# Kernel optimization log

Measured on AMD Instinct MI355X. Metric: run time of the kernel, lower is better.

The kernel has to match this reference:

```python
import jax, jax.numpy as jnp
import numpy as np

V = 50257      # vocab_size
EMB = 300      # emb_size
H = 512        # mcan_flat_out_size (GRU hidden)
HS = 256       # hidden_size (object proposal feature dim)
BH = 256       # bi_hidden_size (encoder output feature dim)
NP = 256       # num_proposal
ML = 50        # max_length (lang seq len)
AL = 20        # answer length -> 19 decode steps
NEG = -1e9


def setup_inputs() -> dict:
    key = jax.random.key(0)
    ks = jax.random.split(key, 30)
    s = 0.02
    n = lambda k, sh: (s * jax.random.normal(k, sh)).astype(jnp.float32)
    d = {}
    d["input_tok"] = jax.random.randint(ks[0], (1,), 0, V, dtype=jnp.int32)
    d["hidden"] = jax.random.normal(ks[1], (1, 1, H), jnp.float32)
    d["encoder_outputs"] = jax.random.normal(ks[2], (ML, BH), jnp.float32)
    d["object_proposals"] = jax.random.normal(ks[3], (NP, HS), jnp.float32)
    d["object_mask"] = jax.random.randint(ks[4], (1, NP), 0, 2, dtype=jnp.int32)
    d["lang_mask"] = jax.random.randint(ks[5], (1, ML), 0, 2, dtype=jnp.int32)
    d["answer_to_vocab"] = jax.random.randint(ks[6], (AL,), 0, V, dtype=jnp.int32)
    # learned params (dropout treated as eval/identity)
    d["emb"] = n(ks[7], (V, EMB))
    cin = H + EMB  # 812
    d["attn_w1"] = n(ks[8], (256, cin)); d["attn_b1"] = jnp.zeros((256,), jnp.float32)
    d["attn_w2"] = n(ks[9], (ML, 256)); d["attn_b2"] = jnp.zeros((ML,), jnp.float32)
    d["attn_op_w1"] = n(ks[10], (256, cin)); d["attn_op_b1"] = jnp.zeros((256,), jnp.float32)
    d["attn_op_w2"] = n(ks[11], (NP, 256)); d["attn_op_b2"] = jnp.zeros((NP,), jnp.float32)
    comb_in = HS + BH + EMB  # 812
    d["cmb_w1"] = n(ks[12], (512, comb_in)); d["cmb_b1"] = jnp.zeros((512,), jnp.float32)
    d["cmb_w2"] = n(ks[13], (H, 512)); d["cmb_b2"] = jnp.zeros((H,), jnp.float32)
    d["gru_w_ih"] = n(ks[14], (3 * H, H)); d["gru_w_hh"] = n(ks[15], (3 * H, H))
    d["gru_b_ih"] = jnp.zeros((3 * H,), jnp.float32); d["gru_b_hh"] = jnp.zeros((3 * H,), jnp.float32)
    d["out_w"] = n(ks[16], (V, H)); d["out_b"] = jnp.zeros((V,), jnp.float32)
    return d


def reference(input_tok, hidden, encoder_outputs, object_proposals, object_mask,
              lang_mask, answer_to_vocab, emb, attn_w1, attn_b1, attn_w2, attn_b2,
              attn_op_w1, attn_op_b1, attn_op_w2, attn_op_b2, cmb_w1, cmb_b1,
              cmb_w2, cmb_b2, gru_w_ih, gru_w_hh, gru_b_ih, gru_b_hh, out_w, out_b):
    obj_m = object_mask.astype(bool)   # [1, NP]
    lang_m = lang_mask.astype(bool)    # [1, ML]
    # teacher forcing: step i embeds answer_to_vocab[i] (step 0 uses input_tok)
    tokens = jnp.concatenate([input_tok, answer_to_vocab[1:-1]])  # [AL-1]

    def step(h, tok):
        # h: [1,1,H]
        x = jax.nn.relu(emb[tok])[None, :]                     # [1,EMB]
        cat = jnp.concatenate([x, h[0]], axis=1)               # [1, EMB+H]
        # object attention
        a_op = jax.nn.relu(cat @ attn_op_w1.T + attn_op_b1) @ attn_op_w2.T + attn_op_b2
        a_op = jax.nn.softmax(jnp.where(obj_m, NEG, a_op), axis=1)   # [1,NP]
        ctx_op = a_op @ object_proposals                       # [1,HS]
        # language attention
        a_l = jax.nn.relu(cat @ attn_w1.T + attn_b1) @ attn_w2.T + attn_b2
        a_l = jax.nn.softmax(jnp.where(lang_m, NEG, a_l), axis=1)    # [1,ML]
        ctx = a_l @ encoder_outputs                            # [1,BH]
        comb = jnp.concatenate([x, ctx, ctx_op], axis=1)       # [1, EMB+BH+HS]
        g = jax.nn.relu(jax.nn.relu(comb @ cmb_w1.T + cmb_b1) @ cmb_w2.T + cmb_b2)  # [1,H]
        # GRU cell (torch gate order: r, z, n)
        gi = g @ gru_w_ih.T + gru_b_ih
        gh = h[0] @ gru_w_hh.T + gru_b_hh
        i_r, i_z, i_n = jnp.split(gi, 3, axis=1)
        h_r, h_z, h_n = jnp.split(gh, 3, axis=1)
        r = jax.nn.sigmoid(i_r + h_r)
        z = jax.nn.sigmoid(i_z + h_z)
        nn_ = jnp.tanh(i_n + r * h_n)
        h_new = (1.0 - z) * nn_ + z * h[0]                     # [1,H]
        logits = h_new @ out_w.T + out_b                       # [1,V]
        return h_new[None], (logits, a_l, a_op)

    _, (logits, attn_w, attn_ob_w) = jax.lax.scan(step, hidden, tokens)
    # logits: [AL-1,1,V]; attn_w: [AL-1,1,ML]; attn_ob_w: [AL-1,1,NP]
    return logits, attn_w, attn_ob_w
```

## Files before the change

### kernel.cpp

```cpp
#include <hip/hip_runtime.h>
#include <math.h>

#define T_STEPS 19
#define V 50257
#define EMB 300
#define HDIM 512
#define NP 256
#define ML 50
#define CIN 812
#define NEGV -1e9f
#define NBLK 64

#define OFF_X      0
#define OFF_POP    5700
#define OFF_PL     10564
#define OFF_PC     15428
#define OFF_HS     25156
#define OFF_H1OP   35396
#define OFF_H1L    35652
#define OFF_C1     35908
#define OFF_G      36420
#define OFF_LOGOP  36932
#define OFF_LOGL   37188
#define OFF_MPROP  37252
#define OFF_MENC   168324
#define OFF_BAR    193924

#define OUT_LOGITS 0
#define OUT_ATTW   ((long)T_STEPS * V)
#define OUT_ATTOB  (OUT_ATTW + (long)T_STEPS * ML)

__device__ __forceinline__ float wred(float v) {
  v += __shfl_xor(v, 32, 64);
  v += __shfl_xor(v, 16, 64);
  v += __shfl_xor(v, 8, 64);
  v += __shfl_xor(v, 4, 64);
  v += __shfl_xor(v, 2, 64);
  v += __shfl_xor(v, 1, 64);
  return v;
}

__device__ __forceinline__ float dot4(float4 a, float4 b) {
  return a.x * b.x + a.y * b.y + a.z * b.z + a.w * b.w;
}

__device__ __forceinline__ void gstore(float* p, float v) {
  __hip_atomic_store(p, v, __ATOMIC_RELAXED, __HIP_MEMORY_SCOPE_AGENT);
}
__device__ __forceinline__ float ld1c(const float* p) {
  return __hip_atomic_load(p, __ATOMIC_RELAXED, __HIP_MEMORY_SCOPE_AGENT);
}
__device__ __forceinline__ float2 ld2c(const float* p) {
  unsigned long long u = __hip_atomic_load((const unsigned long long*)p,
                                           __ATOMIC_RELAXED, __HIP_MEMORY_SCOPE_AGENT);
  float2 r;
  r.x = __uint_as_float((unsigned)u);
  r.y = __uint_as_float((unsigned)(u >> 32));
  return r;
}
__device__ __forceinline__ float4 ld4c(const float* p) {
  float2 a = ld2c(p), b = ld2c(p + 2);
  return make_float4(a.x, a.y, b.x, b.y);
}

__device__ __forceinline__ void gbar(float* wsb, unsigned bar) {
  asm volatile("s_waitcnt vmcnt(0)" ::: "memory");
  __syncthreads();
  unsigned* flags = (unsigned*)(wsb + OFF_BAR) + 16;
  if (threadIdx.x == 0) {
    __hip_atomic_store(flags + 16 * blockIdx.x, bar, __ATOMIC_RELAXED, __HIP_MEMORY_SCOPE_AGENT);
  }
  asm volatile("" ::: "memory");
  if (threadIdx.x < 64) {
    unsigned* f = flags + 16 * threadIdx.x;
    while (__hip_atomic_load(f, __ATOMIC_RELAXED, __HIP_MEMORY_SCOPE_AGENT) < bar) {
      __builtin_amdgcn_s_sleep(1);
    }
  }
  __syncthreads();
}

__global__ void k_pre1(const int* __restrict__ tok0, const int* __restrict__ ans,
                       const float* __restrict__ emb, const float* __restrict__ hidden,
                       float* __restrict__ ws) {
  int tid = blockIdx.x * 256 + threadIdx.x;
  if (tid < T_STEPS * EMB) {
    int s = tid / EMB, j = tid - s * EMB;
    int t = (s == 0) ? tok0[0] : ans[s];
    float v = emb[(long)t * EMB + j];
    ws[OFF_X + tid] = v > 0.f ? v : 0.f;
  } else {
    int k = tid - T_STEPS * EMB;
    if (k < HDIM) ws[OFF_HS + k] = hidden[k];
  }
}

__global__ void k_pre2(const float* __restrict__ w1op, const float* __restrict__ b1op,
                       const float* __restrict__ w1l,  const float* __restrict__ b1l,
                       const float* __restrict__ wc1,  const float* __restrict__ bc1,
                       float* __restrict__ ws) {
  int gw = (blockIdx.x * 256 + threadIdx.x) >> 6;
  int lane = threadIdx.x & 63;
  int s = gw >> 10;
  int rr = gw & 1023;
  if (s >= T_STEPS) return;
  const float* wrow; const float* bias; float* dst; int r;
  if (rr < 256)      { r = rr;       wrow = w1op + (long)r * CIN; bias = b1op; dst = ws + OFF_POP + s * 256 + r; }
  else if (rr < 512) { r = rr - 256; wrow = w1l  + (long)r * CIN; bias = b1l;  dst = ws + OFF_PL  + s * 256 + r; }
  else               { r = rr - 512; wrow = wc1  + (long)r * CIN; bias = bc1;  dst = ws + OFF_PC  + s * 512 + r; }
  const float* x = ws + OFF_X + s * EMB;
  float acc = 0.f;
#pragma unroll
  for (int it = 0; it < 5; ++it) {
    int j = it * 64 + lane;
    if (j < EMB) acc += wrow[j] * x[j];
  }
  acc = wred(acc);
  if (lane == 0) *dst = acc + bias[r];
}

#define LDSF 12850
__global__ void __launch_bounds__(256) k_mprep(const float* __restrict__ cw1,
                                               const float* __restrict__ prop,
                                               const float* __restrict__ enc,
                                               float* __restrict__ ws) {
  __shared__ float lds[LDSF];
  int tid = threadIdx.x, r = blockIdx.x;
  float acc = 0.f;
  for (int kc = 0; kc < 8; ++kc) {
    __syncthreads();
#pragma unroll
    for (int i = 0; i < 8; ++i) {
      int f = tid + 256 * i; int row = f >> 3, q = f & 7;
      float4 v = *(const float4*)(prop + (long)row * 256 + kc * 32 + 4 * q);
      float* p = lds + row * 33 + 4 * q;
      p[0] = v.x; p[1] = v.y; p[2] = v.z; p[3] = v.w;
    }
    __syncthreads();
    const float* wbase = cw1 + (long)r * CIN + 556 + kc * 32;
    const float* pl = lds + tid * 33;
#pragma unroll
    for (int k4 = 0; k4 < 8; ++k4) {
      float4 w4 = *(const float4*)(wbase + 4 * k4);
      const float* pp = pl + 4 * k4;
      acc += w4.x * pp[0] + w4.y * pp[1] + w4.z * pp[2] + w4.w * pp[3];
    }
  }
  ws[OFF_MPROP + (long)r * 256 + tid] = acc;
  __syncthreads();
  for (int i = 0; i < 13; ++i) {
    int f = tid + 256 * i;
    if (f < 3200) {
      int row = f >> 6, q = f & 63;
      float4 v = *(const float4*)(enc + (long)row * 256 + 4 * q);
      float* p = lds + row * 257 + 4 * q;
      p[0] = v.x; p[1] = v.y; p[2] = v.z; p[3] = v.w;
    }
  }
  __syncthreads();
  if (tid < ML) {
    const float* wb2 = cw1 + (long)r * CIN + 300;
    const float* el = lds + tid * 257;
    float a2 = 0.f;
#pragma unroll 8
    for (int k = 0; k < 256; ++k) a2 += wb2[k] * el[k];
    ws[OFF_MENC + (long)r * ML + tid] = a2;
  }
}

__global__ void __launch_bounds__(256, 1) k_recur(
    const float* __restrict__ w1op, const float* __restrict__ w1l,
    const float* __restrict__ whh,  const float* __restrict__ bhh,
    const float* __restrict__ w2op, const float* __restrict__ b2op,
    const float* __restrict__ w2l,  const float* __restrict__ b2l,
    const int* __restrict__ obj_mask, const int* __restrict__ lang_mask,
    const float* __restrict__ wc2,  const float* __restrict__ bc2,
    const float* __restrict__ wih,  const float* __restrict__ bih,
    float* ws, float* __restrict__ out) {
  const int tid = threadIdx.x;
  const int lane = tid & 63;
  const int wv = (blockIdx.x << 2) + (tid >> 6);
  const int r0 = 2 * wv, r1 = 2 * wv + 1;
  const int l4 = 4 * lane;
  unsigned bar = 1;
  __shared__ float red[256];
  __shared__ __align__(16) float sm_aop[256];
  __shared__ float sm_al[64];

  const float* wa0p = (r0 < 256) ? (w1op + (long)r0 * CIN + 300) : (w1l + (long)(r0 - 256) * CIN + 300);
  const float* wa1p = (r1 < 256) ? (w1op + (long)r1 * CIN + 300) : (w1l + (long)(r1 - 256) * CIN + 300);
  float4 WA00 = *(const float4*)(wa0p + l4), WA01 = *(const float4*)(wa0p + 256 + l4);
  float4 WA10 = *(const float4*)(wa1p + l4), WA11 = *(const float4*)(wa1p + 256 + l4);
  const float* q;
  q = whh + (long)r0 * HDIM;           float4 WH00 = *(const float4*)(q + l4), WH01 = *(const float4*)(q + 256 + l4);
  q = whh + (long)(r0 + 512) * HDIM;   float4 WH10 = *(const float4*)(q + l4), WH11 = *(const float4*)(q + 256 + l4);
  q = whh + (long)(r0 + 1024) * HDIM;  float4 WH20 = *(const float4*)(q + l4), WH21 = *(const float4*)(q + 256 + l4);
  q = whh + (long)r1 * HDIM;           float4 WH30 = *(const float4*)(q + l4), WH31 = *(const float4*)(q + 256 + l4);
  q = whh + (long)(r1 + 512) * HDIM;   float4 WH40 = *(const float4*)(q + l4), WH41 = *(const float4*)(q + 256 + l4);
  q = whh + (long)(r1 + 1024) * HDIM;  float4 WH50 = *(const float4*)(q + l4), WH51 = *(const float4*)(q + 256 + l4);
  float4 W2  = *(const float4*)(w2op + (long)wv * 256 + l4);
  float4 W2L = (wv < ML) ? *(const float4*)(w2l + (long)wv * 256 + l4) : make_float4(0.f, 0.f, 0.f, 0.f);
  float4 MP0 = *(const float4*)(ws + OFF_MPROP + (long)r0 * 256 + l4);
  float4 MP1 = *(const float4*)(ws + OFF_MPROP + (long)r1 * 256 + l4);
  float  ME0 = (lane < ML) ? ws[OFF_MENC + (long)r0 * ML + lane] : 0.f;
  float  ME1 = (lane < ML) ? ws[OFF_MENC + (long)r1 * ML + lane] : 0.f;
  q = wc2 + (long)r0 * HDIM;           float4 WC00 = *(const float4*)(q + l4), WC01 = *(const float4*)(q + 256 + l4);
  q = wc2 + (long)r1 * HDIM;           float4 WC10 = *(const float4*)(q + l4), WC11 = *(const float4*)(q + 256 + l4);
  q = wih + (long)r0 * HDIM;           float4 WI00 = *(const float4*)(q + l4), WI01 = *(const float4*)(q + 256 + l4);
  q = wih + (long)(r0 + 512) * HDIM;   float4 WI10 = *(const float4*)(q + l4), WI11 = *(const float4*)(q + 256 + l4);
  q = wih + (long)(r0 + 1024) * HDIM;  float4 WI20 = *(const float4*)(q + l4), WI21 = *(const float4*)(q + 256 + l4);
  q = wih + (long)r1 * HDIM;           float4 WI30 = *(const float4*)(q + l4), WI31 = *(const float4*)(q + 256 + l4);
  q = wih + (long)(r1 + 512) * HDIM;   float4 WI40 = *(const float4*)(q + l4), WI41 = *(const float4*)(q + 256 + l4);
  q = wih + (long)(r1 + 1024) * HDIM;  float4 WI50 = *(const float4*)(q + l4), WI51 = *(const float4*)(q + 256 + l4);
  float BH0 = bhh[r0], BH1 = bhh[512 + r0], BH2 = bhh[1024 + r0];
  float BH3 = bhh[r1], BH4 = bhh[512 + r1], BH5 = bhh[1024 + r1];
  float BI0 = bih[r0], BI1 = bih[512 + r0], BI2 = bih[1024 + r0];
  float BI3 = bih[r1], BI4 = bih[512 + r1], BI5 = bih[1024 + r1];
  float BC0 = bc2[r0], BC1 = bc2[r1];
  float B2  = b2op[wv];
  float B2Lv = (wv < ML) ? b2l[wv] : 0.f;

  for (int s = 0; s < T_STEPS; ++s) {
    float ghr0, ghz0, ghn0, ghr1, ghz1, ghn1;
    {
      const float* h = ws + OFF_HS + s * HDIM;
      float4 ha = ld4c(h + l4);
      float4 hb = ld4c(h + 256 + l4);
      float a0 = dot4(WA00, ha) + dot4(WA01, hb);
      float a1 = dot4(WA10, ha) + dot4(WA11, hb);
      float b0 = dot4(WH00, ha) + dot4(WH01, hb);
      float b1 = dot4(WH10, ha) + dot4(WH11, hb);
      float b2 = dot4(WH20, ha) + dot4(WH21, hb);
      float b3 = dot4(WH30, ha) + dot4(WH31, hb);
      float b4 = dot4(WH40, ha) + dot4(WH41, hb);
      float b5 = dot4(WH50, ha) + dot4(WH51, hb);
      a0 = wred(a0); a1 = wred(a1);
      b0 = wred(b0); b1 = wred(b1); b2 = wred(b2);
      b3 = wred(b3); b4 = wred(b4); b5 = wred(b5);
      ghr0 = b0 + BH0; ghz0 = b1 + BH1; ghn0 = b2 + BH2;
      ghr1 = b3 + BH3; ghz1 = b4 + BH4; ghn1 = b5 + BH5;
      if (lane == 0) {
        float v0 = a0 + ((r0 < 256) ? ws[OFF_POP + s * 256 + r0] : ws[OFF_PL + s * 256 + (r0 - 256)]);
        float v1 = a1 + ((r1 < 256) ? ws[OFF_POP + s * 256 + r1] : ws[OFF_PL + s * 256 + (r1 - 256)]);
        float* d0 = (r0 < 256) ? (ws + OFF_H1OP + r0) : (ws + OFF_H1L + (r0 - 256));
        float* d1 = (r1 < 256) ? (ws + OFF_H1OP + r1) : (ws + OFF_H1L + (r1 - 256));
        gstore(d0, v0 > 0.f ? v0 : 0.f);
        gstore(d1, v1 > 0.f ? v1 : 0.f);
      }
    }
    gbar(ws, bar++);
    {
      float4 h1 = ld4c(ws + OFF_H1OP + l4);
      float acc = wred(dot4(W2, h1));
      if (lane == 0) gstore(ws + OFF_LOGOP + wv, acc + B2);
      if (wv < ML) {
        float4 h1l = ld4c(ws + OFF_H1L + l4);
        float accl = wred(dot4(W2L, h1l));
        if (lane == 0) gstore(ws + OFF_LOGL + wv, accl + B2Lv);
      }
    }
    gbar(ws, bar++);
    {
      float lv = ld1c(ws + OFF_LOGOP + tid);
      float vo = (obj_mask[tid] != 0) ? NEGV : lv;
      red[tid] = vo; __syncthreads();
      for (int st = 128; st > 0; st >>= 1) { if (tid < st) red[tid] = fmaxf(red[tid], red[tid + st]); __syncthreads(); }
      float mo = red[0]; __syncthreads();
      float eo = expf(vo - mo);
      red[tid] = eo; __syncthreads();
      for (int st = 128; st > 0; st >>= 1) { if (tid < st) red[tid] += red[tid + st]; __syncthreads(); }
      float aop = eo / red[0];
      sm_aop[tid] = aop;
      __syncthreads();
      float ll = 0.f;
      if (tid < ML) ll = ld1c(ws + OFF_LOGL + tid);
      float vl = (tid < ML) ? ((lang_mask[tid] != 0) ? NEGV : ll) : -3e38f;
      red[tid] = vl; __syncthreads();
      for (int st = 128; st > 0; st >>= 1) { if (tid < st) red[tid] = fmaxf(red[tid], red[tid + st]); __syncthreads(); }
      float ml_ = red[0]; __syncthreads();
      float el = (tid < ML) ? expf(vl - ml_) : 0.f;
      red[tid] = el; __syncthreads();
      for (int st = 128; st > 0; st >>= 1) { if (tid < st) red[tid] += red[tid + st]; __syncthreads(); }
      float al = el / red[0];
      if (tid < 64) sm_al[tid] = (tid < ML) ? al : 0.f;
      __syncthreads();
      if (blockIdx.x == 0) {
        out[OUT_ATTOB + (long)s * NP + tid] = aop;
        if (tid < ML) out[OUT_ATTW + (long)s * ML + tid] = al;
      }
      float4 a4 = *(const float4*)(&sm_aop[l4]);
      float acc0 = dot4(MP0, a4);
      float acc1 = dot4(MP1, a4);
      if (lane < ML) {
        float alv = sm_al[lane];
        acc0 += ME0 * alv;
        acc1 += ME1 * alv;
      }
      acc0 = wred(acc0); acc1 = wred(acc1);
      if (lane == 0) {
        float v0 = acc0 + ws[OFF_PC + s * HDIM + r0];
        float v1 = acc1 + ws[OFF_PC + s * HDIM + r1];
        gstore(ws + OFF_C1 + r0, v0 > 0.f ? v0 : 0.f);
        gstore(ws + OFF_C1 + r1, v1 > 0.f ? v1 : 0.f);
      }
    }
    gbar(ws, bar++);
    {
      float4 ca = ld4c(ws + OFF_C1 + l4);
      float4 cb = ld4c(ws + OFF_C1 + 256 + l4);
      float acc0 = dot4(WC00, ca) + dot4(WC01, cb);
      float acc1 = dot4(WC10, ca) + dot4(WC11, cb);
      acc0 = wred(acc0); acc1 = wred(acc1);
      if (lane == 0) {
        float v0 = acc0 + BC0;
        float v1 = acc1 + BC1;
        gstore(ws + OFF_G + r0, v0 > 0.f ? v0 : 0.f);
        gstore(ws + OFF_G + r1, v1 > 0.f ? v1 : 0.f);
      }
    }
    gbar(ws, bar++);
    {
      float4 ga = ld4c(ws + OFF_G + l4);
      float4 gb = ld4c(ws + OFF_G + 256 + l4);
      float a0 = dot4(WI00, ga) + dot4(WI01, gb);
      float a1 = dot4(WI10, ga) + dot4(WI11, gb);
      float a2 = dot4(WI20, ga) + dot4(WI21, gb);
      float a3 = dot4(WI30, ga) + dot4(WI31, gb);
      float a4_ = dot4(WI40, ga) + dot4(WI41, gb);
      float a5 = dot4(WI50, ga) + dot4(WI51, gb);
      a0 = wred(a0); a1 = wred(a1); a2 = wred(a2);
      a3 = wred(a3); a4_ = wred(a4_); a5 = wred(a5);
      if (lane == 0) {
        float ir0 = a0 + BI0, iz0 = a1 + BI1, in0 = a2 + BI2;
        float rg0 = 1.f / (1.f + expf(-(ir0 + ghr0)));
        float zg0 = 1.f / (1.f + expf(-(iz0 + ghz0)));
        float ng0 = tanhf(in0 + rg0 * ghn0);
        float hp0 = ld1c(ws + OFF_HS + s * HDIM + r0);
        gstore(ws + OFF_HS + (s + 1) * HDIM + r0, (1.f - zg0) * ng0 + zg0 * hp0);
        float ir1 = a3 + BI3, iz1 = a4_ + BI4, in1 = a5 + BI5;
        float rg1 = 1.f / (1.f + expf(-(ir1 + ghr1)));
        float zg1 = 1.f / (1.f + expf(-(iz1 + ghz1)));
        float ng1 = tanhf(in1 + rg1 * ghn1);
        float hp1 = ld1c(ws + OFF_HS + s * HDIM + r1);
        gstore(ws + OFF_HS + (s + 1) * HDIM + r1, (1.f - zg1) * ng1 + zg1 * hp1);
      }
    }
    gbar(ws, bar++);
  }
}

#define WL(row, q) ((q) * 1032 + 4 * (row))
__global__ void __launch_bounds__(256) k_final2(const float* __restrict__ ow,
                                                const float* __restrict__ ob,
                                                const float* __restrict__ ws,
                                                float* __restrict__ out) {
  __shared__ __align__(16) float wl[8 * 1032];
  __shared__ __align__(16) float hl[T_STEPS * 512];
  int tid = threadIdx.x;
  long rbase = (long)blockIdx.x * 256;
  for (int i = tid; i < T_STEPS * 512; i += 256) hl[i] = ws[OFF_HS + 512 + i];
  float4 st[8];
#pragma unroll
  for (int i = 0; i < 8; ++i) {
    int f = tid + 256 * i; int row = f >> 3, q = f & 7;
    long r = rbase + row;
    st[i] = (r < V) ? *(const float4*)(ow + r * 512 + 4 * q) : make_float4(0.f, 0.f, 0.f, 0.f);
  }
  float acc[T_STEPS];
#pragma unroll
  for (int s = 0; s < T_STEPS; ++s) acc[s] = 0.f;
  __syncthreads();
  for (int c = 0; c < 16; ++c) {
#pragma unroll
    for (int i = 0; i < 8; ++i) {
      int f = tid + 256 * i; int row = f >> 3, q = f & 7;
      *(float4*)(&wl[WL(row, q)]) = st[i];
    }
    __syncthreads();
    if (c < 15) {
#pragma unroll
      for (int i = 0; i < 8; ++i) {
        int f = tid + 256 * i; int row = f >> 3, q = f & 7;
        long r = rbase + row;
        st[i] = (r < V) ? *(const float4*)(ow + r * 512 + (c + 1) * 32 + 4 * q) : make_float4(0.f, 0.f, 0.f, 0.f);
      }
    }
#pragma unroll
    for (int kq = 0; kq < 8; ++kq) {
      float4 w4 = *(const float4*)(&wl[WL(tid, kq)]);
      const float* hb = hl + c * 32 + 4 * kq;
#pragma unroll
      for (int s = 0; s < T_STEPS; ++s) {
        float4 h4 = *(const float4*)(hb + s * 512);
        acc[s] += dot4(w4, h4);
      }
    }
    __syncthreads();
  }
  long r = rbase + tid;
  if (r < V) {
    float b = ob[r];
#pragma unroll
    for (int s = 0; s < T_STEPS; ++s) out[OUT_LOGITS + (long)s * V + r] = acc[s] + b;
  }
}

extern "C" void kernel_launch(void* const* d_in, const int* in_sizes, int n_in,
                              void* d_out, int out_size, void* d_ws, size_t ws_size,
                              hipStream_t stream) {
  const int*   input_tok  = (const int*)d_in[0];
  const float* hidden     = (const float*)d_in[1];
  const float* enc        = (const float*)d_in[2];
  const float* prop       = (const float*)d_in[3];
  const int*   obj_mask   = (const int*)d_in[4];
  const int*   lang_mask  = (const int*)d_in[5];
  const int*   ans        = (const int*)d_in[6];
  const float* emb        = (const float*)d_in[7];
  const float* attn_w1    = (const float*)d_in[8];
  const float* attn_b1    = (const float*)d_in[9];
  const float* attn_w2    = (const float*)d_in[10];
  const float* attn_b2    = (const float*)d_in[11];
  const float* attn_op_w1 = (const float*)d_in[12];
  const float* attn_op_b1 = (const float*)d_in[13];
  const float* attn_op_w2 = (const float*)d_in[14];
  const float* attn_op_b2 = (const float*)d_in[15];
  const float* cmb_w1     = (const float*)d_in[16];
  const float* cmb_b1     = (const float*)d_in[17];
  const float* cmb_w2     = (const float*)d_in[18];
  const float* cmb_b2     = (const float*)d_in[19];
  const float* gw_ih      = (const float*)d_in[20];
  const float* gw_hh      = (const float*)d_in[21];
  const float* gb_ih      = (const float*)d_in[22];
  const float* gb_hh      = (const float*)d_in[23];
  const float* out_w      = (const float*)d_in[24];
  const float* out_b      = (const float*)d_in[25];
  float* out = (float*)d_out;
  float* ws  = (float*)d_ws;

  hipMemsetAsync((char*)d_ws + (size_t)OFF_BAR * 4, 0, 4608, stream);
  k_pre1<<<25, 256, 0, stream>>>(input_tok, ans, emb, hidden, ws);
  k_pre2<<<4864, 256, 0, stream>>>(attn_op_w1, attn_op_b1, attn_w1, attn_b1, cmb_w1, cmb_b1, ws);
  k_mprep<<<512, 256, 0, stream>>>(cmb_w1, prop, enc, ws);
  k_recur<<<NBLK, 256, 0, stream>>>(attn_op_w1, attn_w1, gw_hh, gb_hh,
                                    attn_op_w2, attn_op_b2, attn_w2, attn_b2,
                                    obj_mask, lang_mask, cmb_w2, cmb_b2,
                                    gw_ih, gb_ih, ws, out);
  k_final2<<<(V + 255) / 256, 256, 0, stream>>>(out_w, out_b, ws, out);
}
```

Measured before the change: 412.4 us.

## Replace grid barriers with NaN-poisoned dataflow polling and widen vocab projection tiles

The persistent recurrence kernel no longer uses a flag-based global barrier between phases. Each per-step intermediate gets its own slot in workspace, pre-filled with NaN by a memset. One wave per block polls that slot until no NaN remains, then relays the values into double-buffered LDS for the rest of the block, so blocks wait only for their data instead of every block. The final logits kernel is also changed so each block computes 512 vocab rows with two accumulator sets, using a padded row-major LDS layout. This halves the block count and reuses each hidden-state load for two rows, at the cost of more registers and a larger per-step workspace.

Measured after the change: 568.3 us. 1.38x slower.

```diff
diff --git a/kernel.cpp b/kernel.cpp
--- a/kernel.cpp
+++ b/kernel.cpp
@@ -15,16 +15,24 @@
 #define OFF_POP    5700
 #define OFF_PL     10564
 #define OFF_PC     15428
-#define OFF_HS     25156
-#define OFF_H1OP   35396
-#define OFF_H1L    35652
-#define OFF_C1     35908
-#define OFF_G      36420
-#define OFF_LOGOP  36932
-#define OFF_LOGL   37188
-#define OFF_MPROP  37252
-#define OFF_MENC   168324
-#define OFF_BAR    193924
+#define OFF_MPROP  25156
+#define OFF_MENC   156228
+#define OFF_HS     181828
+#define OFF_H1OP   192068
+#define OFF_H1L    196932
+#define OFF_LOGOP  201796
+#define OFF_LOGL   206660
+#define OFF_C1     207876
+#define OFF_G      217604
+#define POISON_END 227332
+#define POISON_BYTES ((POISON_END - OFF_HS) * 4)
+
+#define H1OP_S(s) (OFF_H1OP + (s) * 256)
+#define H1L_S(s)  (OFF_H1L  + (s) * 256)
+#define LOGOP_S(s)(OFF_LOGOP+ (s) * 256)
+#define LOGL_S(s) (OFF_LOGL + (s) * 64)
+#define C1_S(s)   (OFF_C1   + (s) * 512)
+#define G_S(s)    (OFF_G    + (s) * 512)
 
 #define OUT_LOGITS 0
 #define OUT_ATTW   ((long)T_STEPS * V)
@@ -63,21 +71,37 @@
   return make_float4(a.x, a.y, b.x, b.y);
 }
 
-__device__ __forceinline__ void gbar(float* wsb, unsigned bar) {
-  asm volatile("s_waitcnt vmcnt(0)" ::: "memory");
-  __syncthreads();
-  unsigned* flags = (unsigned*)(wsb + OFF_BAR) + 16;
-  if (threadIdx.x == 0) {
-    __hip_atomic_store(flags + 16 * blockIdx.x, bar, __ATOMIC_RELAXED, __HIP_MEMORY_SCOPE_AGENT);
-  }
-  asm volatile("" ::: "memory");
-  if (threadIdx.x < 64) {
-    unsigned* f = flags + 16 * threadIdx.x;
-    while (__hip_atomic_load(f, __ATOMIC_RELAXED, __HIP_MEMORY_SCOPE_AGENT) < bar) {
-      __builtin_amdgcn_s_sleep(1);
-    }
-  }
-  __syncthreads();
+__device__ __forceinline__ int nan4(float4 v) {
+  return (v.x != v.x) | (v.y != v.y) | (v.z != v.z) | (v.w != v.w);
+}
+__device__ __forceinline__ float4 poll4(const float* p) {
+  float4 v = ld4c(p);
+  while (__any(nan4(v))) { __builtin_amdgcn_s_sleep(1); v = ld4c(p); }
+  return v;
+}
+__device__ __forceinline__ float poll1p(const float* p, bool pred) {
+  float v = pred ? ld1c(p) : 0.f;
+  while (__any(pred & (v != v))) { __builtin_amdgcn_s_sleep(1); if (pred) v = ld1c(p); }
+  return pred ? v : 0.f;
+}
+
+__device__ __forceinline__ void relay512(const float* src, float* ibuf, int lane) {
+  float4 v0 = poll4(src + 8 * lane);
+  float4 v1 = poll4(src + 8 * lane + 4);
+  *(float4*)&ibuf[8 * lane] = v0;
+  *(float4*)&ibuf[8 * lane + 4] = v1;
+}
+__device__ __forceinline__ void relay2x256(const float* a, const float* b, float* ibuf, int lane) {
+  float4 v0 = poll4(a + 4 * lane);
+  float4 v1 = poll4(b + 4 * lane);
+  *(float4*)&ibuf[4 * lane] = v0;
+  *(float4*)&ibuf[256 + 4 * lane] = v1;
+}
+__device__ __forceinline__ void relay256p50(const float* a, const float* b, float* ibuf, int lane) {
+  float4 v0 = poll4(a + 4 * lane);
+  *(float4*)&ibuf[4 * lane] = v0;
+  float v1 = poll1p(b + lane, lane < ML);
+  ibuf[256 + lane] = v1;
 }
 
 __global__ void k_pre1(const int* __restrict__ tok0, const int* __restrict__ ans,
@@ -179,13 +203,14 @@
     float* ws, float* __restrict__ out) {
   const int tid = threadIdx.x;
   const int lane = tid & 63;
+  const bool w0 = (tid < 64);
   const int wv = (blockIdx.x << 2) + (tid >> 6);
   const int r0 = 2 * wv, r1 = 2 * wv + 1;
   const int l4 = 4 * lane;
-  unsigned bar = 1;
   __shared__ float red[256];
   __shared__ __align__(16) float sm_aop[256];
   __shared__ float sm_al[64];
+  __shared__ __align__(16) float ibufs[2][512];
 
   const float* wa0p = (r0 < 256) ? (w1op + (long)r0 * CIN + 300) : (w1l + (long)(r0 - 256) * CIN + 300);
   const float* wa1p = (r1 < 256) ? (w1op + (long)r1 * CIN + 300) : (w1l + (long)(r1 - 256) * CIN + 300);
@@ -220,12 +245,16 @@
   float B2  = b2op[wv];
   float B2Lv = (wv < ML) ? b2l[wv] : 0.f;
 
+  int ph = 0;
+  if (w0) relay512(ws + OFF_HS, ibufs[0], lane);
+
   for (int s = 0; s < T_STEPS; ++s) {
     float ghr0, ghz0, ghn0, ghr1, ghz1, ghn1;
     {
-      const float* h = ws + OFF_HS + s * HDIM;
-      float4 ha = ld4c(h + l4);
-      float4 hb = ld4c(h + 256 + l4);
+      const float* ib = ibufs[ph & 1];
+      __syncthreads();
+      float4 ha = *(const float4*)&ib[l4];
+      float4 hb = *(const float4*)&ib[256 + l4];
       float a0 = dot4(WA00, ha) + dot4(WA01, hb);
       float a1 = dot4(WA10, ha) + dot4(WA11, hb);
       float b0 = dot4(WH00, ha) + dot4(WH01, hb);
@@ -242,26 +271,32 @@
       if (lane == 0) {
         float v0 = a0 + ((r0 < 256) ? ws[OFF_POP + s * 256 + r0] : ws[OFF_PL + s * 256 + (r0 - 256)]);
         float v1 = a1 + ((r1 < 256) ? ws[OFF_POP + s * 256 + r1] : ws[OFF_PL + s * 256 + (r1 - 256)]);
-        float* d0 = (r0 < 256) ? (ws + OFF_H1OP + r0) : (ws + OFF_H1L + (r0 - 256));
-        float* d1 = (r1 < 256) ? (ws + OFF_H1OP + r1) : (ws + OFF_H1L + (r1 - 256));
+        float* d0 = (r0 < 256) ? (ws + H1OP_S(s) + r0) : (ws + H1L_S(s) + (r0 - 256));
+        float* d1 = (r1 < 256) ? (ws + H1OP_S(s) + r1) : (ws + H1L_S(s) + (r1 - 256));
         gstore(d0, v0 > 0.f ? v0 : 0.f);
         gstore(d1, v1 > 0.f ? v1 : 0.f);
       }
-    }
-    gbar(ws, bar++);
+      if (w0) relay2x256(ws + H1OP_S(s), ws + H1L_S(s), ibufs[(ph + 1) & 1], lane);
+      ph++;
+    }
     {
-      float4 h1 = ld4c(ws + OFF_H1OP + l4);
+      const float* ib = ibufs[ph & 1];
+      __syncthreads();
+      float4 h1 = *(const float4*)&ib[l4];
       float acc = wred(dot4(W2, h1));
-      if (lane == 0) gstore(ws + OFF_LOGOP + wv, acc + B2);
+      if (lane == 0) gstore(ws + LOGOP_S(s) + wv, acc + B2);
       if (wv < ML) {
-        float4 h1l = ld4c(ws + OFF_H1L + l4);
+        float4 h1l = *(const float4*)&ib[256 + l4];
         float accl = wred(dot4(W2L, h1l));
-        if (lane == 0) gstore(ws + OFF_LOGL + wv, accl + B2Lv);
-      }
-    }
-    gbar(ws, bar++);
+        if (lane == 0) gstore(ws + LOGL_S(s) + wv, accl + B2Lv);
+      }
+      if (w0) relay256p50(ws + LOGOP_S(s), ws + LOGL_S(s), ibufs[(ph + 1) & 1], lane);
+      ph++;
+    }
     {
-      float lv = ld1c(ws + OFF_LOGOP + tid);
+      const float* ib = ibufs[ph & 1];
+      __syncthreads();
+      float lv = ib[tid];
       float vo = (obj_mask[tid] != 0) ? NEGV : lv;
       red[tid] = vo; __syncthreads();
       for (int st = 128; st > 0; st >>= 1) { if (tid < st) red[tid] = fmaxf(red[tid], red[tid + st]); __syncthreads(); }
@@ -272,8 +307,7 @@
       float aop = eo / red[0];
       sm_aop[tid] = aop;
       __syncthreads();
-      float ll = 0.f;
-      if (tid < ML) ll = ld1c(ws + OFF_LOGL + tid);
+      float ll = (tid < ML) ? ib[256 + tid] : 0.f;
       float vl = (tid < ML) ? ((lang_mask[tid] != 0) ? NEGV : ll) : -3e38f;
       red[tid] = vl; __syncthreads();
       for (int st = 128; st > 0; st >>= 1) { if (tid < st) red[tid] = fmaxf(red[tid], red[tid + st]); __syncthreads(); }
@@ -300,28 +334,34 @@
       if (lane == 0) {
         float v0 = acc0 + ws[OFF_PC + s * HDIM + r0];
         float v1 = acc1 + ws[OFF_PC + s * HDIM + r1];
-        gstore(ws + OFF_C1 + r0, v0 > 0.f ? v0 : 0.f);
-        gstore(ws + OFF_C1 + r1, v1 > 0.f ? v1 : 0.f);
-      }
-    }
-    gbar(ws, bar++);
+        gstore(ws + C1_S(s) + r0, v0 > 0.f ? v0 : 0.f);
+        gstore(ws + C1_S(s) + r1, v1 > 0.f ? v1 : 0.f);
+      }
+      if (w0) relay512(ws + C1_S(s), ibufs[(ph + 1) & 1], lane);
+      ph++;
+    }
     {
-      float4 ca = ld4c(ws + OFF_C1 + l4);
-      float4 cb = ld4c(ws + OFF_C1 + 256 + l4);
+      const float* ib = ibufs[ph & 1];
+      __syncthreads();
+      float4 ca = *(const float4*)&ib[l4];
+      float4 cb = *(const float4*)&ib[256 + l4];
       float acc0 = dot4(WC00, ca) + dot4(WC01, cb);
       float acc1 = dot4(WC10, ca) + dot4(WC11, cb);
       acc0 = wred(acc0); acc1 = wred(acc1);
       if (lane == 0) {
         float v0 = acc0 + BC0;
         float v1 = acc1 + BC1;
-        gstore(ws + OFF_G + r0, v0 > 0.f ? v0 : 0.f);
-        gstore(ws + OFF_G + r1, v1 > 0.f ? v1 : 0.f);
-      }
-    }
-    gbar(ws, bar++);
+        gstore(ws + G_S(s) + r0, v0 > 0.f ? v0 : 0.f);
+        gstore(ws + G_S(s) + r1, v1 > 0.f ? v1 : 0.f);
+      }
+      if (w0) relay512(ws + G_S(s), ibufs[(ph + 1) & 1], lane);
+      ph++;
+    }
     {
-      float4 ga = ld4c(ws + OFF_G + l4);
-      float4 gb = ld4c(ws + OFF_G + 256 + l4);
+      const float* ib = ibufs[ph & 1];
+      __syncthreads();
+      float4 ga = *(const float4*)&ib[l4];
+      float4 gb = *(const float4*)&ib[256 + l4];
       float a0 = dot4(WI00, ga) + dot4(WI01, gb);
       float a1 = dot4(WI10, ga) + dot4(WI11, gb);
       float a2 = dot4(WI20, ga) + dot4(WI21, gb);
@@ -344,42 +384,43 @@
         float hp1 = ld1c(ws + OFF_HS + s * HDIM + r1);
         gstore(ws + OFF_HS + (s + 1) * HDIM + r1, (1.f - zg1) * ng1 + zg1 * hp1);
       }
-    }
-    gbar(ws, bar++);
-  }
-}
-
-#define WL(row, q) ((q) * 1032 + 4 * (row))
-__global__ void __launch_bounds__(256) k_final2(const float* __restrict__ ow,
+      if (w0 && (s + 1 < T_STEPS)) relay512(ws + OFF_HS + (s + 1) * HDIM, ibufs[(ph + 1) & 1], lane);
+      ph++;
+    }
+  }
+}
+
+#define WP 36
+__global__ void __launch_bounds__(256) k_final3(const float* __restrict__ ow,
                                                 const float* __restrict__ ob,
                                                 const float* __restrict__ ws,
                                                 float* __restrict__ out) {
-  __shared__ __align__(16) float wl[8 * 1032];
+  __shared__ __align__(16) float wl[512 * WP];
   __shared__ __align__(16) float hl[T_STEPS * 512];
   int tid = threadIdx.x;
-  long rbase = (long)blockIdx.x * 256;
+  long rbase = (long)blockIdx.x * 512;
   for (int i = tid; i < T_STEPS * 512; i += 256) hl[i] = ws[OFF_HS + 512 + i];
-  float4 st[8];
-#pragma unroll
-  for (int i = 0; i < 8; ++i) {
+  float4 st[16];
+#pragma unroll
+  for (int i = 0; i < 16; ++i) {
     int f = tid + 256 * i; int row = f >> 3, q = f & 7;
     long r = rbase + row;
     st[i] = (r < V) ? *(const float4*)(ow + r * 512 + 4 * q) : make_float4(0.f, 0.f, 0.f, 0.f);
   }
-  float acc[T_STEPS];
-#pragma unroll
-  for (int s = 0; s < T_STEPS; ++s) acc[s] = 0.f;
+  float acc0[T_STEPS], acc1[T_STEPS];
+#pragma unroll
+  for (int s = 0; s < T_STEPS; ++s) { acc0[s] = 0.f; acc1[s] = 0.f; }
   __syncthreads();
   for (int c = 0; c < 16; ++c) {
 #pragma unroll
-    for (int i = 0; i < 8; ++i) {
+    for (int i = 0; i < 16; ++i) {
       int f = tid + 256 * i; int row = f >> 3, q = f & 7;
-      *(float4*)(&wl[WL(row, q)]) = st[i];
+      *(float4*)(&wl[row * WP + 4 * q]) = st[i];
     }
     __syncthreads();
     if (c < 15) {
 #pragma unroll
-      for (int i = 0; i < 8; ++i) {
+      for (int i = 0; i < 16; ++i) {
         int f = tid + 256 * i; int row = f >> 3, q = f & 7;
         long r = rbase + row;
         st[i] = (r < V) ? *(const float4*)(ow + r * 512 + (c + 1) * 32 + 4 * q) : make_float4(0.f, 0.f, 0.f, 0.f);
@@ -387,21 +428,29 @@
     }
 #pragma unroll
     for (int kq = 0; kq < 8; ++kq) {
-      float4 w4 = *(const float4*)(&wl[WL(tid, kq)]);
+      float4 w4a = *(const float4*)(&wl[tid * WP + 4 * kq]);
+      float4 w4b = *(const float4*)(&wl[(tid + 256) * WP + 4 * kq]);
       const float* hb = hl + c * 32 + 4 * kq;
 #pragma unroll
       for (int s = 0; s < T_STEPS; ++s) {
         float4 h4 = *(const float4*)(hb + s * 512);
-        acc[s] += dot4(w4, h4);
+        acc0[s] += dot4(w4a, h4);
+        acc1[s] += dot4(w4b, h4);
       }
     }
     __syncthreads();
   }
-  long r = rbase + tid;
-  if (r < V) {
-    float b = ob[r];
-#pragma unroll
-    for (int s = 0; s < T_STEPS; ++s) out[OUT_LOGITS + (long)s * V + r] = acc[s] + b;
+  long ra = rbase + tid;
+  if (ra < V) {
+    float b = ob[ra];
+#pragma unroll
+    for (int s = 0; s < T_STEPS; ++s) out[OUT_LOGITS + (long)s * V + ra] = acc0[s] + b;
+  }
+  long rb = rbase + 256 + tid;
+  if (rb < V) {
+    float b = ob[rb];
+#pragma unroll
+    for (int s = 0; s < T_STEPS; ++s) out[OUT_LOGITS + (long)s * V + rb] = acc1[s] + b;
   }
 }
 
@@ -437,7 +486,7 @@
   float* out = (float*)d_out;
   float* ws  = (float*)d_ws;
 
-  hipMemsetAsync((char*)d_ws + (size_t)OFF_BAR * 4, 0, 4608, stream);
+  hipMemsetAsync((char*)d_ws + (size_t)OFF_HS * 4, 0xFF, POISON_BYTES, stream);
   k_pre1<<<25, 256, 0, stream>>>(input_tok, ans, emb, hidden, ws);
   k_pre2<<<4864, 256, 0, stream>>>(attn_op_w1, attn_op_b1, attn_w1, attn_b1, cmb_w1, cmb_b1, ws);
   k_mprep<<<512, 256, 0, stream>>>(cmb_w1, prop, enc, ws);
@@ -445,5 +494,5 @@
                                     attn_op_w2, attn_op_b2, attn_w2, attn_b2,
                                     obj_mask, lang_mask, cmb_w2, cmb_b2,
                                     gw_ih, gb_ih, ws, out);
-  k_final2<<<(V + 255) / 256, 256, 0, stream>>>(out_w, out_b, ws, out);
-}
+  k_final3<<<(V + 511) / 512, 256, 0, stream>>>(out_w, out_b, ws, out);
+}
```

## Compute attention logits redundantly per block to drop a grid barrier; split-K output GEMV

Applied to the files above, without the earlier changes.

Each block of the recurrent kernel now computes all second-layer attention logits itself from a pre-transposed copy of the w2 weights, made once by a new prep kernel. This removes one grid-wide barrier per decode step. In exchange every block reads the full 256x256 (and 50x256) weights from global or cache each step. Separately, the final vocabulary projection is split in half along K across 198 blocks, each computing 512 rows. A new combine kernel adds the partial sums and the bias, which costs an extra round trip over the logits array.

After: 673.3 us. 63.3% more time.

```diff
diff --git a/kernel.cpp b/kernel.cpp
--- a/kernel.cpp
+++ b/kernel.cpp
@@ -20,11 +20,12 @@
 #define OFF_H1L    35652
 #define OFF_C1     35908
 #define OFF_G      36420
-#define OFF_LOGOP  36932
-#define OFF_LOGL   37188
-#define OFF_MPROP  37252
-#define OFF_MENC   168324
-#define OFF_BAR    193924
+#define OFF_MPROP  36932
+#define OFF_MENC   168004
+#define OFF_W2OPT  193604
+#define OFF_W2LT   259140
+#define OFF_BAR    275524
+#define OFF_PART   276608
 
 #define OUT_LOGITS 0
 #define OUT_ATTW   ((long)T_STEPS * V)
@@ -168,11 +169,18 @@
   }
 }
 
+__global__ void k_pre4(const float* __restrict__ w2op, const float* __restrict__ w2l,
+                       float* __restrict__ ws) {
+  int r = blockIdx.x;
+  int k = threadIdx.x;
+  ws[OFF_W2OPT + (k >> 2) * 1024 + r * 4 + (k & 3)] = w2op[(long)r * 256 + k];
+  if (r < ML) ws[OFF_W2LT + (k >> 2) * 256 + r * 4 + (k & 3)] = w2l[(long)r * 256 + k];
+}
+
 __global__ void __launch_bounds__(256, 1) k_recur(
     const float* __restrict__ w1op, const float* __restrict__ w1l,
     const float* __restrict__ whh,  const float* __restrict__ bhh,
-    const float* __restrict__ w2op, const float* __restrict__ b2op,
-    const float* __restrict__ w2l,  const float* __restrict__ b2l,
+    const float* __restrict__ b2op, const float* __restrict__ b2l,
     const int* __restrict__ obj_mask, const int* __restrict__ lang_mask,
     const float* __restrict__ wc2,  const float* __restrict__ bc2,
     const float* __restrict__ wih,  const float* __restrict__ bih,
@@ -186,6 +194,8 @@
   __shared__ float red[256];
   __shared__ __align__(16) float sm_aop[256];
   __shared__ float sm_al[64];
+  __shared__ __align__(16) float sm_h1op[256];
+  __shared__ __align__(16) float sm_h1l[256];
 
   const float* wa0p = (r0 < 256) ? (w1op + (long)r0 * CIN + 300) : (w1l + (long)(r0 - 256) * CIN + 300);
   const float* wa1p = (r1 < 256) ? (w1op + (long)r1 * CIN + 300) : (w1l + (long)(r1 - 256) * CIN + 300);
@@ -198,8 +208,6 @@
   q = whh + (long)r1 * HDIM;           float4 WH30 = *(const float4*)(q + l4), WH31 = *(const float4*)(q + 256 + l4);
   q = whh + (long)(r1 + 512) * HDIM;   float4 WH40 = *(const float4*)(q + l4), WH41 = *(const float4*)(q + 256 + l4);
   q = whh + (long)(r1 + 1024) * HDIM;  float4 WH50 = *(const float4*)(q + l4), WH51 = *(const float4*)(q + 256 + l4);
-  float4 W2  = *(const float4*)(w2op + (long)wv * 256 + l4);
-  float4 W2L = (wv < ML) ? *(const float4*)(w2l + (long)wv * 256 + l4) : make_float4(0.f, 0.f, 0.f, 0.f);
   float4 MP0 = *(const float4*)(ws + OFF_MPROP + (long)r0 * 256 + l4);
   float4 MP1 = *(const float4*)(ws + OFF_MPROP + (long)r1 * 256 + l4);
   float  ME0 = (lane < ML) ? ws[OFF_MENC + (long)r0 * ML + lane] : 0.f;
@@ -217,8 +225,6 @@
   float BI0 = bih[r0], BI1 = bih[512 + r0], BI2 = bih[1024 + r0];
   float BI3 = bih[r1], BI4 = bih[512 + r1], BI5 = bih[1024 + r1];
   float BC0 = bc2[r0], BC1 = bc2[r1];
-  float B2  = b2op[wv];
-  float B2Lv = (wv < ML) ? b2l[wv] : 0.f;
 
   for (int s = 0; s < T_STEPS; ++s) {
     float ghr0, ghz0, ghn0, ghr1, ghz1, ghn1;
@@ -250,19 +256,29 @@
     }
     gbar(ws, bar++);
     {
-      float4 h1 = ld4c(ws + OFF_H1OP + l4);
-      float acc = wred(dot4(W2, h1));
-      if (lane == 0) gstore(ws + OFF_LOGOP + wv, acc + B2);
-      if (wv < ML) {
-        float4 h1l = ld4c(ws + OFF_H1L + l4);
-        float accl = wred(dot4(W2L, h1l));
-        if (lane == 0) gstore(ws + OFF_LOGL + wv, accl + B2Lv);
-      }
-    }
-    gbar(ws, bar++);
-    {
-      float lv = ld1c(ws + OFF_LOGOP + tid);
-      float vo = (obj_mask[tid] != 0) ? NEGV : lv;
+      sm_h1op[tid] = ld1c(ws + OFF_H1OP + tid);
+      sm_h1l[tid]  = ld1c(ws + OFF_H1L + tid);
+      __syncthreads();
+      float lo = b2op[tid];
+      const float* w2T = ws + OFF_W2OPT;
+#pragma unroll 8
+      for (int k4 = 0; k4 < 64; ++k4) {
+        float4 h4 = *(const float4*)(&sm_h1op[4 * k4]);
+        float4 w4 = *(const float4*)(&w2T[k4 * 1024 + tid * 4]);
+        lo += dot4(w4, h4);
+      }
+      float llg = 0.f;
+      if (tid < ML) {
+        llg = b2l[tid];
+        const float* wlT = ws + OFF_W2LT;
+#pragma unroll 8
+        for (int k4 = 0; k4 < 64; ++k4) {
+          float4 h4 = *(const float4*)(&sm_h1l[4 * k4]);
+          float4 w4 = *(const float4*)(&wlT[k4 * 256 + tid * 4]);
+          llg += dot4(w4, h4);
+        }
+      }
+      float vo = (obj_mask[tid] != 0) ? NEGV : lo;
       red[tid] = vo; __syncthreads();
       for (int st = 128; st > 0; st >>= 1) { if (tid < st) red[tid] = fmaxf(red[tid], red[tid + st]); __syncthreads(); }
       float mo = red[0]; __syncthreads();
@@ -272,9 +288,7 @@
       float aop = eo / red[0];
       sm_aop[tid] = aop;
       __syncthreads();
-      float ll = 0.f;
-      if (tid < ML) ll = ld1c(ws + OFF_LOGL + tid);
-      float vl = (tid < ML) ? ((lang_mask[tid] != 0) ? NEGV : ll) : -3e38f;
+      float vl = (tid < ML) ? ((lang_mask[tid] != 0) ? NEGV : llg) : -3e38f;
       red[tid] = vl; __syncthreads();
       for (int st = 128; st > 0; st >>= 1) { if (tid < st) red[tid] = fmaxf(red[tid], red[tid + st]); __syncthreads(); }
       float ml_ = red[0]; __syncthreads();
@@ -350,58 +364,85 @@
 }
 
 #define WL(row, q) ((q) * 1032 + 4 * (row))
-__global__ void __launch_bounds__(256) k_final2(const float* __restrict__ ow,
-                                                const float* __restrict__ ob,
+__global__ void __launch_bounds__(256) k_final4(const float* __restrict__ ow,
                                                 const float* __restrict__ ws,
                                                 float* __restrict__ out) {
-  __shared__ __align__(16) float wl[8 * 1032];
-  __shared__ __align__(16) float hl[T_STEPS * 512];
+  __shared__ __align__(16) float wla[8 * 1032];
+  __shared__ __align__(16) float wlb[8 * 1032];
+  __shared__ __align__(16) float hl[T_STEPS * 256];
   int tid = threadIdx.x;
-  long rbase = (long)blockIdx.x * 256;
-  for (int i = tid; i < T_STEPS * 512; i += 256) hl[i] = ws[OFF_HS + 512 + i];
-  float4 st[8];
-#pragma unroll
-  for (int i = 0; i < 8; ++i) {
+  int half = blockIdx.x / 99;
+  int rblk = blockIdx.x - 99 * half;
+  long rbase = (long)rblk * 512;
+  int kbase = half * 256;
+  for (int i = tid; i < T_STEPS * 256; i += 256) {
+    int s = i >> 8, k = i & 255;
+    hl[i] = ws[OFF_HS + 512 + s * 512 + kbase + k];
+  }
+  float4 st[16];
+#pragma unroll
+  for (int i = 0; i < 16; ++i) {
     int f = tid + 256 * i; int row = f >> 3, q = f & 7;
     long r = rbase + row;
-    st[i] = (r < V) ? *(const float4*)(ow + r * 512 + 4 * q) : make_float4(0.f, 0.f, 0.f, 0.f);
-  }
-  float acc[T_STEPS];
-#pragma unroll
-  for (int s = 0; s < T_STEPS; ++s) acc[s] = 0.f;
+    st[i] = (r < V) ? *(const float4*)(ow + r * 512 + kbase + 4 * q) : make_float4(0.f, 0.f, 0.f, 0.f);
+  }
+  float acc0[T_STEPS], acc1[T_STEPS];
+#pragma unroll
+  for (int s = 0; s < T_STEPS; ++s) { acc0[s] = 0.f; acc1[s] = 0.f; }
   __syncthreads();
-  for (int c = 0; c < 16; ++c) {
+  for (int c = 0; c < 8; ++c) {
 #pragma unroll
     for (int i = 0; i < 8; ++i) {
       int f = tid + 256 * i; int row = f >> 3, q = f & 7;
-      *(float4*)(&wl[WL(row, q)]) = st[i];
+      *(float4*)(&wla[WL(row, q)]) = st[i];
+    }
+#pragma unroll
+    for (int i = 8; i < 16; ++i) {
+      int f = tid + 256 * i; int row = (f >> 3) - 256, q = f & 7;
+      *(float4*)(&wlb[WL(row, q)]) = st[i];
     }
     __syncthreads();
-    if (c < 15) {
-#pragma unroll
-      for (int i = 0; i < 8; ++i) {
+    if (c < 7) {
+#pragma unroll
+      for (int i = 0; i < 16; ++i) {
         int f = tid + 256 * i; int row = f >> 3, q = f & 7;
         long r = rbase + row;
-        st[i] = (r < V) ? *(const float4*)(ow + r * 512 + (c + 1) * 32 + 4 * q) : make_float4(0.f, 0.f, 0.f, 0.f);
+        st[i] = (r < V) ? *(const float4*)(ow + r * 512 + kbase + (c + 1) * 32 + 4 * q) : make_float4(0.f, 0.f, 0.f, 0.f);
       }
     }
 #pragma unroll
     for (int kq = 0; kq < 8; ++kq) {
-      float4 w4 = *(const float4*)(&wl[WL(tid, kq)]);
+      float4 w4a = *(const float4*)(&wla[WL(tid, kq)]);
+      float4 w4b = *(const float4*)(&wlb[WL(tid, kq)]);
       const float* hb = hl + c * 32 + 4 * kq;
 #pragma unroll
       for (int s = 0; s < T_STEPS; ++s) {
-        float4 h4 = *(const float4*)(hb + s * 512);
-        acc[s] += dot4(w4, h4);
+        float4 h4 = *(const float4*)(hb + s * 256);
+        acc0[s] += dot4(w4a, h4);
+        acc1[s] += dot4(w4b, h4);
       }
     }
     __syncthreads();
   }
-  long r = rbase + tid;
-  if (r < V) {
-    float b = ob[r];
-#pragma unroll
-    for (int s = 0; s < T_STEPS; ++s) out[OUT_LOGITS + (long)s * V + r] = acc[s] + b;
+  float* dst = (half == 0) ? (out + OUT_LOGITS) : ((float*)ws + OFF_PART);
+  long ra = rbase + tid;
+  if (ra < V) {
+#pragma unroll
+    for (int s = 0; s < T_STEPS; ++s) dst[(long)s * V + ra] = acc0[s];
+  }
+  long rb = rbase + 256 + tid;
+  if (rb < V) {
+#pragma unroll
+    for (int s = 0; s < T_STEPS; ++s) dst[(long)s * V + rb] = acc1[s];
+  }
+}
+
+__global__ void k_comb(const float* __restrict__ ws, const float* __restrict__ ob,
+                       float* __restrict__ out) {
+  long idx = (long)blockIdx.x * 256 + threadIdx.x;
+  if (idx < (long)T_STEPS * V) {
+    int r = (int)(idx % V);
+    out[OUT_LOGITS + idx] = out[OUT_LOGITS + idx] + ws[OFF_PART + idx] + ob[r];
   }
 }
 
@@ -441,9 +482,11 @@
   k_pre1<<<25, 256, 0, stream>>>(input_tok, ans, emb, hidden, ws);
   k_pre2<<<4864, 256, 0, stream>>>(attn_op_w1, attn_op_b1, attn_w1, attn_b1, cmb_w1, cmb_b1, ws);
   k_mprep<<<512, 256, 0, stream>>>(cmb_w1, prop, enc, ws);
+  k_pre4<<<256, 256, 0, stream>>>(attn_op_w2, attn_w2, ws);
   k_recur<<<NBLK, 256, 0, stream>>>(attn_op_w1, attn_w1, gw_hh, gb_hh,
-                                    attn_op_w2, attn_op_b2, attn_w2, attn_b2,
+                                    attn_op_b2, attn_b2,
                                     obj_mask, lang_mask, cmb_w2, cmb_b2,
                                     gw_ih, gb_ih, ws, out);
-  k_final2<<<(V + 255) / 256, 256, 0, stream>>>(out_w, out_b, ws, out);
-}
+  k_final4<<<198, 256, 0, stream>>>(out_w, ws, out);
+  k_comb<<<(int)(((long)T_STEPS * V + 255) / 256), 256, 0, stream>>>(ws, out_b, out);
+}
```

## Rewrite output projection as wave-per-row dot with wave reductions

Applied to the files above, without the earlier changes.

The vocab projection kernel no longer stages weight tiles through LDS with one thread per row. Each 64-lane wave now takes a whole output row: every lane loads 8 contiguous weights, forms partial dots against all 19 hidden states held in LDS, and the partials are combined with wave reductions. The grid becomes a fixed 1024 blocks striding over rows. This gives coalesced weight loads and drops the LDS tiling and barriers, at the cost of 19 cross-lane reductions per row and scalar stores from lane 0.

Measured after the change: 423.7 us. 1.03x slower.

```diff
diff --git a/kernel.cpp b/kernel.cpp
--- a/kernel.cpp
+++ b/kernel.cpp
@@ -349,59 +349,34 @@
   }
 }
 
-#define WL(row, q) ((q) * 1032 + 4 * (row))
-__global__ void __launch_bounds__(256) k_final2(const float* __restrict__ ow,
+__global__ void __launch_bounds__(256) k_final5(const float* __restrict__ ow,
                                                 const float* __restrict__ ob,
                                                 const float* __restrict__ ws,
                                                 float* __restrict__ out) {
-  __shared__ __align__(16) float wl[8 * 1032];
   __shared__ __align__(16) float hl[T_STEPS * 512];
   int tid = threadIdx.x;
-  long rbase = (long)blockIdx.x * 256;
+  int lane = tid & 63;
   for (int i = tid; i < T_STEPS * 512; i += 256) hl[i] = ws[OFF_HS + 512 + i];
-  float4 st[8];
-#pragma unroll
-  for (int i = 0; i < 8; ++i) {
-    int f = tid + 256 * i; int row = f >> 3, q = f & 7;
-    long r = rbase + row;
-    st[i] = (r < V) ? *(const float4*)(ow + r * 512 + 4 * q) : make_float4(0.f, 0.f, 0.f, 0.f);
-  }
-  float acc[T_STEPS];
-#pragma unroll
-  for (int s = 0; s < T_STEPS; ++s) acc[s] = 0.f;
   __syncthreads();
-  for (int c = 0; c < 16; ++c) {
-#pragma unroll
-    for (int i = 0; i < 8; ++i) {
-      int f = tid + 256 * i; int row = f >> 3, q = f & 7;
-      *(float4*)(&wl[WL(row, q)]) = st[i];
-    }
-    __syncthreads();
-    if (c < 15) {
-#pragma unroll
-      for (int i = 0; i < 8; ++i) {
-        int f = tid + 256 * i; int row = f >> 3, q = f & 7;
-        long r = rbase + row;
-        st[i] = (r < V) ? *(const float4*)(ow + r * 512 + (c + 1) * 32 + 4 * q) : make_float4(0.f, 0.f, 0.f, 0.f);
-      }
-    }
-#pragma unroll
-    for (int kq = 0; kq < 8; ++kq) {
-      float4 w4 = *(const float4*)(&wl[WL(tid, kq)]);
-      const float* hb = hl + c * 32 + 4 * kq;
-#pragma unroll
-      for (int s = 0; s < T_STEPS; ++s) {
-        float4 h4 = *(const float4*)(hb + s * 512);
-        acc[s] += dot4(w4, h4);
-      }
-    }
-    __syncthreads();
-  }
-  long r = rbase + tid;
-  if (r < V) {
-    float b = ob[r];
-#pragma unroll
-    for (int s = 0; s < T_STEPS; ++s) out[OUT_LOGITS + (long)s * V + r] = acc[s] + b;
+  int gwave = (blockIdx.x << 2) + (tid >> 6);
+  int nw = gridDim.x << 2;
+  for (long r = gwave; r < V; r += nw) {
+    const float* wr = ow + r * 512 + 8 * lane;
+    float4 w0 = *(const float4*)(wr);
+    float4 w1 = *(const float4*)(wr + 4);
+    float acc[T_STEPS];
+#pragma unroll
+    for (int s = 0; s < T_STEPS; ++s) {
+      const float* hb = hl + s * 512 + 8 * lane;
+      acc[s] = dot4(w0, *(const float4*)(hb)) + dot4(w1, *(const float4*)(hb + 4));
+    }
+#pragma unroll
+    for (int s = 0; s < T_STEPS; ++s) acc[s] = wred(acc[s]);
+    if (lane == 0) {
+      float b = ob[r];
+#pragma unroll
+      for (int s = 0; s < T_STEPS; ++s) out[OUT_LOGITS + (long)s * V + r] = acc[s] + b;
+    }
   }
 }
 
@@ -445,5 +420,5 @@
                                     attn_op_w2, attn_op_b2, attn_w2, attn_b2,
                                     obj_mask, lang_mask, cmb_w2, cmb_b2,
                                     gw_ih, gb_ih, ws, out);
-  k_final2<<<(V + 255) / 256, 256, 0, stream>>>(out_w, out_b, ws, out);
-}
+  k_final5<<<1024, 256, 0, stream>>>(out_w, out_b, ws, out);
+}
```
